# Kernel optimization log

Measured on AMD Instinct MI355X. Metric: run time of the kernel, lower is better.

Reference implementation:

```python
import jax, jax.numpy as jnp
import numpy as np

# Config constants (match init_kwargs)
E = 16          # n_routed_experts
G = 4           # n_groups
TOPK_G = 2      # topk_groups
K = 4           # n_activated_experts
ROUTE_SCALE = 2.5446


def setup_inputs() -> dict:
    key = jax.random.key(0)
    ks = jax.random.split(key, 9)
    T, D, H = 2048, 1024, 704
    HS = 2 * H  # shared FFN hidden = n_shared_experts * expert_hidden_dim
    sc = lambda k, shape, fan_in: (jax.random.normal(k, shape, jnp.float32)
                                   * (fan_in ** -0.5))
    return {
        "x":      jax.random.normal(ks[0], (T, D), jnp.float32),
        "gate_w": sc(ks[1], (E, D), D),
        "gate_b": jnp.zeros((E,), jnp.float32),       # V3 routing bias (init 0)
        "w1":     sc(ks[2], (E, H, D), D),            # gate proj per expert
        "w3":     sc(ks[3], (E, H, D), D),            # up proj per expert
        "w2":     sc(ks[4], (E, D, H), H),            # down proj per expert
        "ws1":    sc(ks[5], (HS, D), D),              # shared FFN gate proj
        "ws3":    sc(ks[6], (HS, D), D),              # shared FFN up proj
        "ws2":    sc(ks[7], (D, HS), HS),             # shared FFN down proj
    }


def _gate(x, gate_w, gate_b):
    """DeepSeek-V3 sigmoid gate with bias routing + group-limited masking."""
    T = x.shape[0]
    logits = x @ gate_w.T                                   # [T, E]
    scores = jax.nn.sigmoid(logits).astype(jnp.float32)     # original_scores
    routing = scores + gate_b                               # bias only affects routing
    g = routing.reshape(T, G, E // G)
    # use_bias=True -> group score = sum of top-2 routing scores in group
    group_scores = jnp.sum(jax.lax.top_k(g, 2)[0], axis=-1)     # [T, G]
    top_groups = jax.lax.top_k(group_scores, TOPK_G)[1]         # [T, TOPK_G]
    keep = jnp.any(jnp.arange(G)[None, :, None] == top_groups[:, None, :],
                   axis=-1)                                     # [T, G]
    routing = jnp.where(keep[:, :, None], g, -jnp.inf).reshape(T, E)
    idx = jax.lax.top_k(routing, K)[1]                          # [T, K]
    w = jnp.take_along_axis(scores, idx, axis=1)                # un-biased weights
    w = w / jnp.clip(jnp.sum(w, axis=-1, keepdims=True), 1e-9)  # sigmoid renorm
    w = (w * ROUTE_SCALE).astype(x.dtype)
    return w, idx


def reference(x, gate_w, gate_b, w1, w3, w2, ws1, ws3, ws2):
    T, D = x.shape
    weights, idx = _gate(x, gate_w, gate_b)                 # [T,K], [T,K]
    # Dense dispatch/combine matrix: combine[t, e] = gate weight (0 if unrouted)
    combine = jnp.zeros((T, E), x.dtype).at[
        jnp.arange(T)[:, None], idx].add(weights)           # [T, E]
    # Routed experts: SwiGLU per expert, grouped GEMMs
    hg = jnp.einsum('td,ehd->eth', x, w1)                   # [E, T, H]
    hu = jnp.einsum('td,ehd->eth', x, w3)                   # [E, T, H]
    eo = jnp.einsum('eth,edh->etd', jax.nn.silu(hg) * hu, w2)  # [E, T, D]
    y_routed = jnp.einsum('etd,te->td', eo, combine)        # [T, D]
    # Shared experts (always active SwiGLU)
    y_shared = (jax.nn.silu(x @ ws1.T) * (x @ ws3.T)) @ ws2.T
    return y_routed + y_shared
```

## Files before the change

kernel.cpp:

```cpp
#include <hip/hip_runtime.h>
#include <hip/hip_bf16.h>
#include <math.h>

typedef __attribute__((ext_vector_type(4))) float   f32x4;
typedef __attribute__((ext_vector_type(8))) short   short8;
typedef __attribute__((ext_vector_type(8))) __bf16  bf16x8;

union SB8 { short8 s; bf16x8 b; };

__device__ __forceinline__ short f2bf(float f) {
  union { float f; unsigned u; } v; v.f = f;
  unsigned r = v.u + 0x7fffu + ((v.u >> 16) & 1u);
  return (short)(r >> 16);
}

__device__ __forceinline__ short8 cvt8(f32x4 a, f32x4 b) {
  short8 r;
  r[0] = f2bf(a[0]); r[1] = f2bf(a[1]); r[2] = f2bf(a[2]); r[3] = f2bf(a[3]);
  r[4] = f2bf(b[0]); r[5] = f2bf(b[1]); r[6] = f2bf(b[2]); r[7] = f2bf(b[3]);
  return r;
}

__device__ __forceinline__ void ldsload16(const short* g, short* l) {
  __builtin_amdgcn_global_load_lds(
      (const __attribute__((address_space(1))) unsigned int*)g,
      (__attribute__((address_space(3))) unsigned int*)l, 16, 0, 0);
}

#define TT   2048
#define DD   1024
#define HH   704
#define HSS  1408
#define EE   16
#define CAP  2048
#define CSTR 32

#define O1  2097152ULL
#define O2  13631488ULL
#define O3  25165824ULL
#define O4  36700160ULL
#define O5  38141952ULL
#define O6  39583744ULL
#define CVT_TOTAL 41025536ULL

#define W2SZ    11534336ULL
#define WS1SZ   1441792ULL
#define WS1END  26607616ULL
#define CVTA_TOTAL  28049408ULL
#define CVTA_BLOCKS 3424
#define GATE_BLOCKS 512

__global__ __launch_bounds__(256)
void gate_cvt(const float* __restrict__ x,  const float* __restrict__ w1,
              const float* __restrict__ w3, const float* __restrict__ s1,
              const float* __restrict__ s3, short* __restrict__ dst,
              const float* __restrict__ gw, const float* __restrict__ gb,
              int* __restrict__ counts, int* __restrict__ tok,
              float* __restrict__ wgt, int* __restrict__ eslot)
{
  if (blockIdx.x >= GATE_BLOCKS) {
    const int tid = threadIdx.x;
    const size_t base = (size_t)(blockIdx.x - GATE_BLOCKS) * 8192;
    const float* sp[4]; short* dp[4];
    #pragma unroll
    for (int k = 0; k < 4; k++) {
      const size_t sb = base + (size_t)k * 2048;
      const float* src; size_t doff;
      if      (sb < O1)     { src = x  + sb;            doff = sb; }
      else if (sb < O2)     { src = w1 + (sb - O1);     doff = sb; }
      else if (sb < O3)     { src = w3 + (sb - O2);     doff = sb; }
      else if (sb < WS1END) { src = s1 + (sb - O3);     doff = sb + W2SZ; }
      else                  { src = s3 + (sb - WS1END); doff = sb + W2SZ; }
      sp[k] = src + tid * 8;
      dp[k] = dst + doff + tid * 8;
    }
    f32x4 va[8];
    #pragma unroll
    for (int k = 0; k < 4; k++) {
      va[2 * k]     = *(const f32x4*)(sp[k]);
      va[2 * k + 1] = *(const f32x4*)(sp[k] + 4);
    }
    #pragma unroll
    for (int k = 0; k < 4; k++)
      *(short8*)(dp[k]) = cvt8(va[2 * k], va[2 * k + 1]);
    return;
  }

  const int lane = threadIdx.x & 63;
  const int wid  = threadIdx.x >> 6;
  const int t    = blockIdx.x * 4 + wid;
  const int e    = lane & 15;
  const int p    = lane >> 4;

  const float* xp = x + (size_t)t * DD + p * 256;
  const float* gp = gw + (size_t)e * DD + p * 256;

  double a0 = 0.0, a1 = 0.0, a2 = 0.0, a3 = 0.0;
  #pragma unroll 8
  for (int i = 0; i < 64; i++) {
    f32x4 xa = *(const f32x4*)(xp + i * 4);
    f32x4 ga = *(const f32x4*)(gp + i * 4);
    a0 += (double)xa[0] * (double)ga[0];
    a1 += (double)xa[1] * (double)ga[1];
    a2 += (double)xa[2] * (double)ga[2];
    a3 += (double)xa[3] * (double)ga[3];
  }
  double acc = (a0 + a1) + (a2 + a3);
  acc += __shfl_xor(acc, 16);
  acc += __shfl_xor(acc, 32);
  float accf = (float)acc;

  float lf[EE], sc[EE], r[EE];
  #pragma unroll
  for (int j = 0; j < EE; j++) lf[j] = __shfl(accf, j);
  #pragma unroll
  for (int j = 0; j < EE; j++) {
    sc[j] = 1.f / (1.f + expf(-lf[j]));
    r[j] = sc[j] + gb[j];
  }
  float gs[4];
  #pragma unroll
  for (int g = 0; g < 4; g++) {
    float m1 = -1e30f, m2 = -1e30f;
    #pragma unroll
    for (int j = 0; j < 4; j++) {
      float v = r[g * 4 + j];
      if (v > m1) { m2 = m1; m1 = v; }
      else if (v > m2) { m2 = v; }
    }
    gs[g] = m1 + m2;
  }
  int g1 = 0, g2 = -1; float b1 = -1e30f, b2 = -1e30f;
  #pragma unroll
  for (int g = 0; g < 4; g++) {
    if (gs[g] > b1) { b2 = b1; g2 = g1; b1 = gs[g]; g1 = g; }
    else if (gs[g] > b2) { b2 = gs[g]; g2 = g; }
  }
  int idx[4]; float wv[4]; float wsum = 0.f;
  unsigned used = 0;
  #pragma unroll
  for (int k = 0; k < 4; k++) {
    float best = -1e30f; int bi = 0;
    #pragma unroll
    for (int j = 0; j < EE; j++) {
      int g = j >> 2;
      bool keep = (g == g1) || (g == g2);
      if (keep && !((used >> j) & 1) && r[j] > best) { best = r[j]; bi = j; }
    }
    used |= 1u << bi; idx[k] = bi; wv[k] = sc[bi]; wsum += sc[bi];
  }
  float div = wsum < 1e-9f ? 1e-9f : wsum;
  if (lane < 4) {
    float w = wv[lane] / div * 2.5446f;
    int slot = atomicAdd(&counts[idx[lane] * CSTR], 1);
    tok[idx[lane] * CAP + slot] = t;
    wgt[idx[lane] * CAP + slot] = w;
    eslot[t * 4 + lane] = (idx[lane] << 16) | slot;
  }
}

__global__ __launch_bounds__(256, 2)
void gemm1_merged(const short* __restrict__ xb, const short* __restrict__ w1b,
                  const short* __restrict__ w3b, const short* __restrict__ ws1b,
                  const short* __restrict__ ws3b, short* __restrict__ act_r,
                  short* __restrict__ act_s, const int* __restrict__ counts,
                  const int* __restrict__ tok,
                  const float* __restrict__ w2f, const float* __restrict__ ws2f,
                  short* __restrict__ w2bd, short* __restrict__ ws2bd)
{
  const int F = blockIdx.x + 11 * (blockIdx.y + 16 * blockIdx.z);
  const int r8 = F & 7, rank = F >> 3;
  int z, Mt, Nt;
  if (rank < 22) {
    z = 0;
    const int p = rank * 8 + r8;
    Mt = p / 11; Nt = p - Mt * 11;
  } else if (rank < 374) {
    const int rr = rank - 22;
    z = 1 + r8 + 8 * (rr / 176);
    const int p = rr % 176;
    Mt = p / 11; Nt = p - Mt * 11;
  } else {
    z = 17;
    const int p = (rank - 374) * 8 + r8;
    Mt = p / 11; Nt = p - Mt * 11;
  }

  if (z == 0) {
    const int bid = Mt * 11 + Nt;
    const int tid = threadIdx.x;
    for (int s = 0; s < 9; s++) {
      const size_t base = (size_t)bid * 73728 + (size_t)s * 8192;
      const float* sp[4]; short* dp[4];
      #pragma unroll
      for (int k = 0; k < 4; k++) {
        const size_t sb = base + (size_t)k * 2048;
        if (sb < W2SZ) {
          sp[k] = w2f + sb + tid * 8;
          dp[k] = w2bd + sb + tid * 8;
        } else {
          const size_t o = sb - W2SZ;
          sp[k] = ws2f + o + tid * 8;
          dp[k] = ws2bd + o + tid * 8;
        }
      }
      f32x4 va[8];
      #pragma unroll
      for (int k = 0; k < 4; k++) {
        va[2 * k]     = *(const f32x4*)(sp[k]);
        va[2 * k + 1] = *(const f32x4*)(sp[k] + 4);
      }
      #pragma unroll
      for (int k = 0; k < 4; k++)
        *(short8*)(dp[k]) = cvt8(va[2 * k], va[2 * k + 1]);
    }
    return;
  }

  const bool routed = (z <= EE);
  const int e = z - 1;

  int cnt, N, rowbase = 0;
  const short *W1, *W3;
  short* act;
  if (routed) {
    if (Nt >= 6) return;
    cnt = counts[e * CSTR];
    if (Mt * 128 >= cnt) return;
    int rb = 0;
    for (int i = 0; i < e; i++) rb += counts[i * CSTR];
    rowbase = rb;
    N = HH;
    W1 = w1b + (size_t)e * HH * DD;
    W3 = w3b + (size_t)e * HH * DD;
    act = act_r;
  } else {
    cnt = TT; N = HSS; W1 = ws1b; W3 = ws3b; act = act_s;
  }

  __shared__ __align__(16) short lA[128 * 64];
  __shared__ __align__(16) short lB1[128 * 64];
  __shared__ __align__(16) short lB3[128 * 64];

  const int tid = threadIdx.x, lane = tid & 63, wv = tid >> 6;
  const int srow = lane >> 3, schunk = lane & 7, scg = schunk ^ srow;

  const short* pa[4]; const short* pb1[4]; const short* pb3[4];
  #pragma unroll
  for (int i = 0; i < 4; i++) {
    const int g = wv * 4 + i;
    int arow = Mt * 128 + g * 8 + srow;
    if (routed) {
      int slot = arow < cnt ? arow : cnt - 1;
      arow = tok[e * CAP + slot];
    }
    pa[i] = xb + (size_t)arow * DD + scg * 8;
    const int brow = Nt * 128 + g * 8 + srow;
    pb1[i] = W1 + (size_t)brow * DD + scg * 8;
    pb3[i] = W3 + (size_t)brow * DD + scg * 8;
  }

  f32x4 acc1[8][2], acc3[8][2];
  #pragma unroll
  for (int i = 0; i < 8; i++) {
    #pragma unroll
    for (int j = 0; j < 2; j++) { acc1[i][j] = (f32x4)0.f; acc3[i][j] = (f32x4)0.f; }
  }

  const int q = lane >> 4, r7 = lane & 7, hi = (lane & 15) >> 3;

  for (int kk = 0; kk < DD; kk += 64) {
    #pragma unroll
    for (int i = 0; i < 4; i++) {
      const int g = wv * 4 + i;
      ldsload16(pa[i] + kk,  lA  + g * 512);
      ldsload16(pb1[i] + kk, lB1 + g * 512);
      ldsload16(pb3[i] + kk, lB3 + g * 512);
    }
    __syncthreads();
    #pragma unroll
    for (int kc = 0; kc < 2; kc++) {
      const int cx = (kc * 4 + q) ^ r7;
      SB8 b1f[2], b3f[2];
      #pragma unroll
      for (int ntl = 0; ntl < 2; ntl++) {
        const int a16 = ((wv * 2 + ntl) * 2 + hi) * 64 + r7 * 8 + cx;
        b1f[ntl].s = *(const short8*)(lB1 + a16 * 8);
        b3f[ntl].s = *(const short8*)(lB3 + a16 * 8);
      }
      #pragma unroll
      for (int mt = 0; mt < 8; mt++) {
        const int a16 = (2 * mt + hi) * 64 + r7 * 8 + cx;
        SB8 af; af.s = *(const short8*)(lA + a16 * 8);
        acc1[mt][0] = __builtin_amdgcn_mfma_f32_16x16x32_bf16(af.b, b1f[0].b, acc1[mt][0], 0, 0, 0);
        acc1[mt][1] = __builtin_amdgcn_mfma_f32_16x16x32_bf16(af.b, b1f[1].b, acc1[mt][1], 0, 0, 0);
        acc3[mt][0] = __builtin_amdgcn_mfma_f32_16x16x32_bf16(af.b, b3f[0].b, acc3[mt][0], 0, 0, 0);
        acc3[mt][1] = __builtin_amdgcn_mfma_f32_16x16x32_bf16(af.b, b3f[1].b, acc3[mt][1], 0, 0, 0);
      }
    }
    __syncthreads();
  }

  const int quad = lane >> 4, lcol = lane & 15;
  #pragma unroll
  for (int mt = 0; mt < 8; mt++) {
    #pragma unroll
    for (int ntl = 0; ntl < 2; ntl++) {
      const int col = Nt * 128 + (wv * 2 + ntl) * 16 + lcol;
      #pragma unroll
      for (int rg = 0; rg < 4; rg++) {
        const int r = Mt * 128 + mt * 16 + quad * 4 + rg;
        if (r < cnt && col < N) {
          float g = acc1[mt][ntl][rg], u = acc3[mt][ntl][rg];
          float a = g / (1.f + __expf(-g)) * u;
          act[(size_t)(rowbase + r) * N + col] = f2bf(a);
        }
      }
    }
  }
}

__global__ __launch_bounds__(256, 2)
void gemm2_merged(const short* __restrict__ act_r, const short* __restrict__ act_s,
                  const short* __restrict__ w2b, const short* __restrict__ ws2b,
                  float* __restrict__ y, float* __restrict__ outr,
                  const int* __restrict__ counts, const float* __restrict__ wgt)
{
  const int F = blockIdx.x + 8 * (blockIdx.y + 16 * blockIdx.z);
  const int r8 = F & 7, rank = F >> 3;
  int z, Mt, Nt;
  if (rank < 256) {
    z = r8 + 8 * (rank >> 7);
    const int p = rank & 127;
    Mt = p >> 3; Nt = p & 7;
  } else {
    z = 16;
    const int p = (rank - 256) * 8 + r8;
    Mt = p >> 3; Nt = p & 7;
  }

  const bool routed = (z < EE);

  int cnt, Kd, rowbase = 0;
  const short *A, *W;
  if (routed) {
    cnt = counts[z * CSTR];
    if (Mt * 128 >= cnt) return;
    int rb = 0;
    for (int i = 0; i < z; i++) rb += counts[i * CSTR];
    rowbase = rb;
    Kd = HH;
    A = act_r + (size_t)rowbase * HH;
    W = w2b + (size_t)z * DD * HH;
  } else {
    cnt = TT; Kd = HSS; A = act_s; W = ws2b;
  }

  __shared__ __align__(16) short lA[128 * 64];
  __shared__ __align__(16) short lB[128 * 64];

  const int tid = threadIdx.x, lane = tid & 63, wv = tid >> 6;
  const int srow = lane >> 3, schunk = lane & 7, scg = schunk ^ srow;

  const short* pa[4]; const short* pb[4];
  #pragma unroll
  for (int i = 0; i < 4; i++) {
    const int g = wv * 4 + i;
    int arow = Mt * 128 + g * 8 + srow;
    if (arow >= cnt) arow = cnt - 1;
    pa[i] = A + (size_t)arow * Kd + scg * 8;
    const int brow = Nt * 128 + g * 8 + srow;
    pb[i] = W + (size_t)brow * Kd + scg * 8;
  }

  f32x4 acc[8][2];
  #pragma unroll
  for (int i = 0; i < 8; i++) { acc[i][0] = (f32x4)0.f; acc[i][1] = (f32x4)0.f; }

  const int q = lane >> 4, r7 = lane & 7, hi = (lane & 15) >> 3;

  for (int kk = 0; kk < Kd; kk += 64) {
    #pragma unroll
    for (int i = 0; i < 4; i++) {
      const int g = wv * 4 + i;
      ldsload16(pa[i] + kk, lA + g * 512);
      ldsload16(pb[i] + kk, lB + g * 512);
    }
    __syncthreads();
    #pragma unroll
    for (int kc = 0; kc < 2; kc++) {
      const int cx = (kc * 4 + q) ^ r7;
      SB8 bf[2];
      #pragma unroll
      for (int ntl = 0; ntl < 2; ntl++) {
        const int a16 = ((wv * 2 + ntl) * 2 + hi) * 64 + r7 * 8 + cx;
        bf[ntl].s = *(const short8*)(lB + a16 * 8);
      }
      #pragma unroll
      for (int mt = 0; mt < 8; mt++) {
        const int a16 = (2 * mt + hi) * 64 + r7 * 8 + cx;
        SB8 af; af.s = *(const short8*)(lA + a16 * 8);
        acc[mt][0] = __builtin_amdgcn_mfma_f32_16x16x32_bf16(af.b, bf[0].b, acc[mt][0], 0, 0, 0);
        acc[mt][1] = __builtin_amdgcn_mfma_f32_16x16x32_bf16(af.b, bf[1].b, acc[mt][1], 0, 0, 0);
      }
    }
    __syncthreads();
  }

  const int quad = lane >> 4, lcol = lane & 15;
  #pragma unroll
  for (int mt = 0; mt < 8; mt++) {
    #pragma unroll
    for (int ntl = 0; ntl < 2; ntl++) {
      const int col = Nt * 128 + (wv * 2 + ntl) * 16 + lcol;
      #pragma unroll
      for (int rg = 0; rg < 4; rg++) {
        const int slot = Mt * 128 + mt * 16 + quad * 4 + rg;
        const float v = acc[mt][ntl][rg];
        if (routed) {
          if (slot < cnt) {
            const float w = wgt[z * CAP + slot];
            outr[(size_t)(rowbase + slot) * DD + col] = w * v;
          }
        } else {
          y[(size_t)slot * DD + col] = v;
        }
      }
    }
  }
}

__global__ __launch_bounds__(256)
void combine_kernel(float* __restrict__ y, const float* __restrict__ outr,
                    const int* __restrict__ eslot, const int* __restrict__ counts)
{
  const int t = blockIdx.x;
  const int d = threadIdx.x * 4;

  int offs[EE];
  int s = 0;
  #pragma unroll
  for (int i = 0; i < EE; i++) { offs[i] = s; s += counts[i * CSTR]; }

  f32x4 accv = *(f32x4*)(y + (size_t)t * DD + d);
  #pragma unroll
  for (int k = 0; k < 4; k++) {
    const int es = eslot[t * 4 + k];
    const int row = offs[es >> 16] + (es & 0xFFFF);
    accv += *(const f32x4*)(outr + (size_t)row * DD + d);
  }
  *(f32x4*)(y + (size_t)t * DD + d) = accv;
}

extern "C" void kernel_launch(void* const* d_in, const int* in_sizes, int n_in,
                              void* d_out, int out_size, void* d_ws, size_t ws_size,
                              hipStream_t stream) {
  const float* x      = (const float*)d_in[0];
  const float* gate_w = (const float*)d_in[1];
  const float* gate_b = (const float*)d_in[2];
  const float* w1     = (const float*)d_in[3];
  const float* w3     = (const float*)d_in[4];
  const float* w2     = (const float*)d_in[5];
  const float* ws1    = (const float*)d_in[6];
  const float* ws3    = (const float*)d_in[7];
  const float* ws2    = (const float*)d_in[8];
  float* y = (float*)d_out;

  char* ws = (char*)d_ws;
  int*   counts = (int*)ws;
  int*   tok    = (int*)(ws + 2048);
  float* wgt    = (float*)(ws + 2048 + (size_t)EE * CAP * 4);
  int*   eslot  = (int*)(ws + 2048 + (size_t)EE * CAP * 8);
  short* bf     = (short*)(ws + 2048 + (size_t)EE * CAP * 8 + (size_t)TT * 16);
  short* xb   = bf;
  short* w1b  = bf + O1;
  short* w3b  = bf + O2;
  short* w2b  = bf + O3;
  short* ws1b = bf + O4;
  short* ws3b = bf + O5;
  short* ws2b = bf + O6;
  short* act_r = bf + CVT_TOTAL;
  short* act_s = act_r + (size_t)8192 * HH;
  float* outr = (float*)(bf + O1);

  (void)hipMemsetAsync(counts, 0, EE * CSTR * sizeof(int), stream);

  gate_cvt<<<GATE_BLOCKS + CVTA_BLOCKS, 256, 0, stream>>>(
      x, w1, w3, ws1, ws3, bf,
      gate_w, gate_b, counts, tok, wgt, eslot);

  gemm1_merged<<<dim3(11, TT / 128, EE + 2), 256, 0, stream>>>(
      xb, w1b, w3b, ws1b, ws3b, act_r, act_s, counts, tok,
      w2, ws2, w2b, ws2b);

  gemm2_merged<<<dim3(DD / 128, TT / 128, EE + 1), 256, 0, stream>>>(
      act_r, act_s, w2b, ws2b, y, outr, counts, wgt);

  combine_kernel<<<TT, 256, 0, stream>>>(y, outr, eslot, counts);
}
```

Before: 301.8 us.

## Double-buffer LDS in both GEMMs and narrow gemm1 N-tile to 64

Both grouped GEMM kernels now use two LDS buffers, issuing global-to-LDS loads for the next K tile before computing the current one. Waits use an explicit vmcnt and raw s_barrier instead of __syncthreads. gemm1 switches from a 128-wide to a 64-wide N tile, so routed experts use 11 column tiles, the shared FFN uses 22, and the grid grows by one z slice. The aim is to hide global memory latency and cut wasted tiles from the N=704 padding, at the cost of doubled LDS footprint (possible occupancy loss) and fiddly vmcnt accounting.

```diff
diff --git a/kernel.cpp b/kernel.cpp
--- a/kernel.cpp
+++ b/kernel.cpp
@@ -159,6 +159,20 @@
   }
 }
 
+#define WAIT_PREV_TILE()  do { \
+    asm volatile("s_waitcnt vmcnt(8)" ::: "memory"); \
+    __builtin_amdgcn_sched_barrier(0); \
+    __builtin_amdgcn_s_barrier(); \
+    __builtin_amdgcn_sched_barrier(0); } while (0)
+#define WAIT_LAST_TILE()  do { \
+    asm volatile("s_waitcnt vmcnt(0)" ::: "memory"); \
+    __builtin_amdgcn_sched_barrier(0); \
+    __builtin_amdgcn_s_barrier(); \
+    __builtin_amdgcn_sched_barrier(0); } while (0)
+#define END_TILE_BARRIER() do { \
+    __builtin_amdgcn_sched_barrier(0); \
+    __builtin_amdgcn_s_barrier(); } while (0)
+
 __global__ __launch_bounds__(256, 2)
 void gemm1_merged(const short* __restrict__ xb, const short* __restrict__ w1b,
                   const short* __restrict__ w3b, const short* __restrict__ ws1b,
@@ -170,24 +184,24 @@
 {
   const int F = blockIdx.x + 11 * (blockIdx.y + 16 * blockIdx.z);
   const int r8 = F & 7, rank = F >> 3;
-  int z, Mt, Nt;
+  int z, Mt, Ntc;
   if (rank < 22) {
     z = 0;
     const int p = rank * 8 + r8;
-    Mt = p / 11; Nt = p - Mt * 11;
+    Mt = p / 11; Ntc = p - Mt * 11;
   } else if (rank < 374) {
     const int rr = rank - 22;
     z = 1 + r8 + 8 * (rr / 176);
     const int p = rr % 176;
-    Mt = p / 11; Nt = p - Mt * 11;
+    Mt = p / 11; Ntc = p - Mt * 11;
   } else {
     z = 17;
     const int p = (rank - 374) * 8 + r8;
-    Mt = p / 11; Nt = p - Mt * 11;
+    Mt = p / 22; Ntc = p - Mt * 22;
   }
 
   if (z == 0) {
-    const int bid = Mt * 11 + Nt;
+    const int bid = Mt * 11 + Ntc;
     const int tid = threadIdx.x;
     for (int s = 0; s < 9; s++) {
       const size_t base = (size_t)bid * 73728 + (size_t)s * 8192;
@@ -224,7 +238,6 @@
   const short *W1, *W3;
   short* act;
   if (routed) {
-    if (Nt >= 6) return;
     cnt = counts[e * CSTR];
     if (Mt * 128 >= cnt) return;
     int rb = 0;
@@ -237,15 +250,16 @@
   } else {
     cnt = TT; N = HSS; W1 = ws1b; W3 = ws3b; act = act_s;
   }
-
-  __shared__ __align__(16) short lA[128 * 64];
-  __shared__ __align__(16) short lB1[128 * 64];
-  __shared__ __align__(16) short lB3[128 * 64];
+  const int NtB = Ntc * 64;
+
+  __shared__ __align__(16) short lA [2][128 * 64];
+  __shared__ __align__(16) short lB1[2][64 * 64];
+  __shared__ __align__(16) short lB3[2][64 * 64];
 
   const int tid = threadIdx.x, lane = tid & 63, wv = tid >> 6;
   const int srow = lane >> 3, schunk = lane & 7, scg = schunk ^ srow;
 
-  const short* pa[4]; const short* pb1[4]; const short* pb3[4];
+  const short* pa[4]; const short* pb1[2]; const short* pb3[2];
   #pragma unroll
   for (int i = 0; i < 4; i++) {
     const int g = wv * 4 + i;
@@ -255,69 +269,68 @@
       arow = tok[e * CAP + slot];
     }
     pa[i] = xb + (size_t)arow * DD + scg * 8;
-    const int brow = Nt * 128 + g * 8 + srow;
+  }
+  #pragma unroll
+  for (int i = 0; i < 2; i++) {
+    const int g = wv * 2 + i;
+    const int brow = NtB + g * 8 + srow;
     pb1[i] = W1 + (size_t)brow * DD + scg * 8;
     pb3[i] = W3 + (size_t)brow * DD + scg * 8;
   }
 
-  f32x4 acc1[8][2], acc3[8][2];
-  #pragma unroll
-  for (int i = 0; i < 8; i++) {
-    #pragma unroll
-    for (int j = 0; j < 2; j++) { acc1[i][j] = (f32x4)0.f; acc3[i][j] = (f32x4)0.f; }
-  }
+  f32x4 acc1[8], acc3[8];
+  #pragma unroll
+  for (int i = 0; i < 8; i++) { acc1[i] = (f32x4)0.f; acc3[i] = (f32x4)0.f; }
 
   const int q = lane >> 4, r7 = lane & 7, hi = (lane & 15) >> 3;
 
-  for (int kk = 0; kk < DD; kk += 64) {
-    #pragma unroll
-    for (int i = 0; i < 4; i++) {
-      const int g = wv * 4 + i;
-      ldsload16(pa[i] + kk,  lA  + g * 512);
-      ldsload16(pb1[i] + kk, lB1 + g * 512);
-      ldsload16(pb3[i] + kk, lB3 + g * 512);
-    }
-    __syncthreads();
-    #pragma unroll
-    for (int kc = 0; kc < 2; kc++) {
-      const int cx = (kc * 4 + q) ^ r7;
-      SB8 b1f[2], b3f[2];
-      #pragma unroll
-      for (int ntl = 0; ntl < 2; ntl++) {
-        const int a16 = ((wv * 2 + ntl) * 2 + hi) * 64 + r7 * 8 + cx;
-        b1f[ntl].s = *(const short8*)(lB1 + a16 * 8);
-        b3f[ntl].s = *(const short8*)(lB3 + a16 * 8);
+#define STAGE1(c, kk) do { \
+    _Pragma("unroll") for (int i = 0; i < 4; i++) \
+      ldsload16(pa[i] + (kk),  &lA [c][(wv * 4 + i) * 512]); \
+    _Pragma("unroll") for (int i = 0; i < 2; i++) { \
+      ldsload16(pb1[i] + (kk), &lB1[c][(wv * 2 + i) * 512]); \
+      ldsload16(pb3[i] + (kk), &lB3[c][(wv * 2 + i) * 512]); } } while (0)
+
+#define GEMM1_BODY(c) do { \
+    _Pragma("unroll") for (int kc = 0; kc < 2; kc++) { \
+      const int cx = (kc * 4 + q) ^ r7; \
+      SB8 b1f, b3f; \
+      b1f.s = *(const short8*)(&lB1[c][((wv * 2 + hi) * 64 + r7 * 8 + cx) * 8]); \
+      b3f.s = *(const short8*)(&lB3[c][((wv * 2 + hi) * 64 + r7 * 8 + cx) * 8]); \
+      _Pragma("unroll") for (int mt = 0; mt < 8; mt++) { \
+        SB8 af; af.s = *(const short8*)(&lA[c][((2 * mt + hi) * 64 + r7 * 8 + cx) * 8]); \
+        acc1[mt] = __builtin_amdgcn_mfma_f32_16x16x32_bf16(af.b, b1f.b, acc1[mt], 0, 0, 0); \
+        acc3[mt] = __builtin_amdgcn_mfma_f32_16x16x32_bf16(af.b, b3f.b, acc3[mt], 0, 0, 0); \
+      } } } while (0)
+
+  STAGE1(0, 0);
+  int cur = 0;
+  for (int kk = 64; kk < DD; kk += 64) {
+    STAGE1(cur ^ 1, kk);
+    WAIT_PREV_TILE();
+    GEMM1_BODY(cur);
+    END_TILE_BARRIER();
+    cur ^= 1;
+  }
+  WAIT_LAST_TILE();
+  GEMM1_BODY(cur);
+
+  const int quad = lane >> 4, lcol = lane & 15;
+  const int col = NtB + wv * 16 + lcol;
+  #pragma unroll
+  for (int mt = 0; mt < 8; mt++) {
+    #pragma unroll
+    for (int rg = 0; rg < 4; rg++) {
+      const int r = Mt * 128 + mt * 16 + quad * 4 + rg;
+      if (r < cnt) {
+        float g = acc1[mt][rg], u = acc3[mt][rg];
+        float a = g / (1.f + __expf(-g)) * u;
+        act[(size_t)(rowbase + r) * N + col] = f2bf(a);
       }
-      #pragma unroll
-      for (int mt = 0; mt < 8; mt++) {
-        const int a16 = (2 * mt + hi) * 64 + r7 * 8 + cx;
-        SB8 af; af.s = *(const short8*)(lA + a16 * 8);
-        acc1[mt][0] = __builtin_amdgcn_mfma_f32_16x16x32_bf16(af.b, b1f[0].b, acc1[mt][0], 0, 0, 0);
-        acc1[mt][1] = __builtin_amdgcn_mfma_f32_16x16x32_bf16(af.b, b1f[1].b, acc1[mt][1], 0, 0, 0);
-        acc3[mt][0] = __builtin_amdgcn_mfma_f32_16x16x32_bf16(af.b, b3f[0].b, acc3[mt][0], 0, 0, 0);
-        acc3[mt][1] = __builtin_amdgcn_mfma_f32_16x16x32_bf16(af.b, b3f[1].b, acc3[mt][1], 0, 0, 0);
-      }
-    }
-    __syncthreads();
-  }
-
-  const int quad = lane >> 4, lcol = lane & 15;
-  #pragma unroll
-  for (int mt = 0; mt < 8; mt++) {
-    #pragma unroll
-    for (int ntl = 0; ntl < 2; ntl++) {
-      const int col = Nt * 128 + (wv * 2 + ntl) * 16 + lcol;
-      #pragma unroll
-      for (int rg = 0; rg < 4; rg++) {
-        const int r = Mt * 128 + mt * 16 + quad * 4 + rg;
-        if (r < cnt && col < N) {
-          float g = acc1[mt][ntl][rg], u = acc3[mt][ntl][rg];
-          float a = g / (1.f + __expf(-g)) * u;
-          act[(size_t)(rowbase + r) * N + col] = f2bf(a);
-        }
-      }
-    }
-  }
+    }
+  }
+#undef STAGE1
+#undef GEMM1_BODY
 }
 
 __global__ __launch_bounds__(256, 2)
@@ -356,8 +369,8 @@
     cnt = TT; Kd = HSS; A = act_s; W = ws2b;
   }
 
-  __shared__ __align__(16) short lA[128 * 64];
-  __shared__ __align__(16) short lB[128 * 64];
+  __shared__ __align__(16) short lA[2][128 * 64];
+  __shared__ __align__(16) short lB[2][128 * 64];
 
   const int tid = threadIdx.x, lane = tid & 63, wv = tid >> 6;
   const int srow = lane >> 3, schunk = lane & 7, scg = schunk ^ srow;
@@ -379,33 +392,38 @@
 
   const int q = lane >> 4, r7 = lane & 7, hi = (lane & 15) >> 3;
 
-  for (int kk = 0; kk < Kd; kk += 64) {
-    #pragma unroll
-    for (int i = 0; i < 4; i++) {
-      const int g = wv * 4 + i;
-      ldsload16(pa[i] + kk, lA + g * 512);
-      ldsload16(pb[i] + kk, lB + g * 512);
-    }
-    __syncthreads();
-    #pragma unroll
-    for (int kc = 0; kc < 2; kc++) {
-      const int cx = (kc * 4 + q) ^ r7;
-      SB8 bf[2];
-      #pragma unroll
-      for (int ntl = 0; ntl < 2; ntl++) {
-        const int a16 = ((wv * 2 + ntl) * 2 + hi) * 64 + r7 * 8 + cx;
-        bf[ntl].s = *(const short8*)(lB + a16 * 8);
-      }
-      #pragma unroll
-      for (int mt = 0; mt < 8; mt++) {
-        const int a16 = (2 * mt + hi) * 64 + r7 * 8 + cx;
-        SB8 af; af.s = *(const short8*)(lA + a16 * 8);
-        acc[mt][0] = __builtin_amdgcn_mfma_f32_16x16x32_bf16(af.b, bf[0].b, acc[mt][0], 0, 0, 0);
-        acc[mt][1] = __builtin_amdgcn_mfma_f32_16x16x32_bf16(af.b, bf[1].b, acc[mt][1], 0, 0, 0);
-      }
-    }
-    __syncthreads();
-  }
+#define STAGE2(c, kk) do { \
+    _Pragma("unroll") for (int i = 0; i < 4; i++) { \
+      const int g = wv * 4 + i; \
+      ldsload16(pa[i] + (kk), &lA[c][g * 512]); \
+      ldsload16(pb[i] + (kk), &lB[c][g * 512]); } } while (0)
+
+#define GEMM2_BODY(c) do { \
+    _Pragma("unroll") for (int kc = 0; kc < 2; kc++) { \
+      const int cx = (kc * 4 + q) ^ r7; \
+      SB8 bf[2]; \
+      _Pragma("unroll") for (int ntl = 0; ntl < 2; ntl++) { \
+        const int a16 = ((wv * 2 + ntl) * 2 + hi) * 64 + r7 * 8 + cx; \
+        bf[ntl].s = *(const short8*)(&lB[c][a16 * 8]); \
+      } \
+      _Pragma("unroll") for (int mt = 0; mt < 8; mt++) { \
+        const int a16 = (2 * mt + hi) * 64 + r7 * 8 + cx; \
+        SB8 af; af.s = *(const short8*)(&lA[c][a16 * 8]); \
+        acc[mt][0] = __builtin_amdgcn_mfma_f32_16x16x32_bf16(af.b, bf[0].b, acc[mt][0], 0, 0, 0); \
+        acc[mt][1] = __builtin_amdgcn_mfma_f32_16x16x32_bf16(af.b, bf[1].b, acc[mt][1], 0, 0, 0); \
+      } } } while (0)
+
+  STAGE2(0, 0);
+  int cur = 0;
+  for (int kk = 64; kk < Kd; kk += 64) {
+    STAGE2(cur ^ 1, kk);
+    WAIT_PREV_TILE();
+    GEMM2_BODY(cur);
+    END_TILE_BARRIER();
+    cur ^= 1;
+  }
+  WAIT_LAST_TILE();
+  GEMM2_BODY(cur);
 
   const int quad = lane >> 4, lcol = lane & 15;
   #pragma unroll
@@ -428,6 +446,8 @@
       }
     }
   }
+#undef STAGE2
+#undef GEMM2_BODY
 }
 
 __global__ __launch_bounds__(256)
@@ -489,7 +509,7 @@
       x, w1, w3, ws1, ws3, bf,
       gate_w, gate_b, counts, tok, wgt, eslot);
 
-  gemm1_merged<<<dim3(11, TT / 128, EE + 2), 256, 0, stream>>>(
+  gemm1_merged<<<dim3(11, TT / 128, EE + 3), 256, 0, stream>>>(
       xb, w1b, w3b, ws1b, ws3b, act_r, act_s, counts, tok,
       w2, ws2, w2b, ws2b);
 
```

Result: slower. 316.5 us (+4.9%).
